# Performance work log

Measured on AMD Instinct MI355X. Metric: run time of the kernel, lower is better.

The kernel has to match this reference:

```python
import jax, jax.numpy as jnp
import numpy as np

BN_EPS = 1e-5
K_HOPS = 10


def setup_inputs() -> dict:
    key = jax.random.key(0)
    ks = jax.random.split(key, 8)
    N, F, H, C, E = 169343, 128, 256, 40, 1200000
    return {
        "x": jax.random.normal(ks[0], (N, F), dtype=jnp.float32),
        "edge_index": jax.random.randint(ks[1], (2, E), 0, N, dtype=jnp.int64),
        "norm": jax.random.uniform(ks[2], (E,), dtype=jnp.float32),
        "W1": jax.random.normal(ks[3], (F, H), dtype=jnp.float32) * (1.0 / np.sqrt(F)),
        "b1": jnp.zeros((H,), jnp.float32),
        "bn_gamma": jnp.ones((H,), jnp.float32),
        "bn_beta": jnp.zeros((H,), jnp.float32),
        "bn_mean": jnp.zeros((H,), jnp.float32),
        "bn_var": jnp.ones((H,), jnp.float32),
        "W2": jax.random.normal(ks[4], (H, C), dtype=jnp.float32) * (1.0 / np.sqrt(H)),
        "b2": jnp.zeros((C,), jnp.float32),
        "proj_w": jax.random.normal(ks[5], (C,), dtype=jnp.float32) * (1.0 / np.sqrt(C)),
        "proj_b": jnp.zeros((1,), jnp.float32),
    }


def reference(x, edge_index, norm, W1, b1, bn_gamma, bn_beta, bn_mean, bn_var,
              W2, b2, proj_w, proj_b):
    N = x.shape[0]
    src, dst = edge_index[0], edge_index[1]

    # MLP head: Linear -> BatchNorm (eval, running stats) -> ReLU -> Linear
    h = x @ W1 + b1
    h = (h - bn_mean) * jax.lax.rsqrt(bn_var + BN_EPS) * bn_gamma + bn_beta
    h = jax.nn.relu(h)  # dropout: identity at inference
    h = h @ W2 + b2  # [N, C]

    # K-hop norm-weighted scatter-add propagation, collecting snapshots
    def hop(carry, _):
        msgs = norm[:, None] * carry[src]              # [E, C]
        nxt = jax.ops.segment_sum(msgs, dst, num_segments=N)
        return nxt, nxt

    _, hops = jax.lax.scan(hop, h, None, length=K_HOPS)  # [K, N, C]
    pps = jnp.concatenate([h[None], hops], axis=0)       # [K+1, N, C]
    pps = jnp.transpose(pps, (1, 0, 2))                  # [N, K+1, C]

    # sigmoid attention over hops, weighted combine
    retain = jax.nn.sigmoid(pps @ proj_w + proj_b[0])    # [N, K+1]
    out = jnp.einsum("nk,nkc->nc", retain, pps)          # [N, C]
    return jax.nn.log_softmax(out, axis=1)
```

## Files before the change

### kernel.cpp

```cpp
#include <hip/hip_runtime.h>
#include <hip/hip_bf16.h>
#include <math.h>

#define F 128
#define H 256
#define C 40
#define KHOPS 10
#define TM 32
#define HK 64

__global__ void k_count(const int* __restrict__ dst, int E, int* __restrict__ cnt) {
    int e = blockIdx.x * 256 + threadIdx.x;
    if (e < E) atomicAdd(&cnt[dst[e]], 1);
}

__global__ void k_scan1(const int* __restrict__ cnt, int n, int* __restrict__ bsum) {
    __shared__ int sh[256];
    int t = threadIdx.x;
    int base = blockIdx.x * 4096 + t * 16;
    int s = 0;
    for (int i = 0; i < 16; i++) { int idx = base + i; if (idx < n) s += cnt[idx]; }
    sh[t] = s; __syncthreads();
    for (int o = 128; o > 0; o >>= 1) {
        if (t < o) sh[t] += sh[t + o];
        __syncthreads();
    }
    if (t == 0) bsum[blockIdx.x] = sh[0];
}

__global__ void k_scan2(int* __restrict__ bsum, int nb) {
    if (threadIdx.x == 0) {
        int acc = 0;
        for (int i = 0; i < nb; i++) { int v = bsum[i]; bsum[i] = acc; acc += v; }
    }
}

__global__ void k_scan3(const int* __restrict__ cnt, int n, const int* __restrict__ bsum,
                        int* __restrict__ rp) {
    __shared__ int sh[256];
    int t = threadIdx.x;
    int base = blockIdx.x * 4096 + t * 16;
    int local[16]; int s = 0;
    for (int i = 0; i < 16; i++) {
        int idx = base + i;
        int v = (idx < n) ? cnt[idx] : 0;
        local[i] = v; s += v;
    }
    sh[t] = s; __syncthreads();
    for (int o = 1; o < 256; o <<= 1) {
        int v = (t >= o) ? sh[t - o] : 0;
        __syncthreads();
        sh[t] += v;
        __syncthreads();
    }
    int excl = (t == 0) ? 0 : sh[t - 1];
    int run = bsum[blockIdx.x] + excl;
    for (int i = 0; i < 16; i++) {
        int idx = base + i;
        if (idx < n) { rp[idx] = run; run += local[i]; }
    }
}

__global__ void k_fill(const int* __restrict__ src, const int* __restrict__ dst,
                       const float* __restrict__ nrm, int E, const int* __restrict__ rp,
                       int* __restrict__ cur, int2* __restrict__ ep) {
    int e = blockIdx.x * 256 + threadIdx.x;
    if (e < E) {
        int d = dst[e];
        int p = rp[d] + atomicAdd(&cur[d], 1);
        ep[p] = make_int2(src[e], __float_as_int(nrm[e]));
    }
}

__launch_bounds__(256, 4)
__global__ void k_mlp(const float* __restrict__ x, const float* __restrict__ W1,
                      const float* __restrict__ b1, const float* __restrict__ g,
                      const float* __restrict__ be, const float* __restrict__ mu,
                      const float* __restrict__ var, const float* __restrict__ W2,
                      const float* __restrict__ b2, const float* __restrict__ pw,
                      const float* __restrict__ pb,
                      float* __restrict__ hbuf, float* __restrict__ oacc, int N) {
    __shared__ float xs[TM][132];
    __shared__ float h1s[TM][68];
    __shared__ float w2s[C][68];
    __shared__ float asc[HK], dsc[HK];
    __shared__ float redc[256];
    __shared__ float sigv[TM];

    int t = threadIdx.x;
    int n0 = blockIdx.x * TM;

    for (int k = 0; k < 4; k++) {
        int idx = k * 256 + t;
        int node = idx >> 5, f4 = idx & 31;
        int n = n0 + node;
        float4 v = (n < N) ? ((const float4*)x)[(size_t)n * (F / 4) + f4]
                           : make_float4(0.f, 0.f, 0.f, 0.f);
        *((float4*)&xs[node][f4 * 4]) = v;
    }

    int n_loc = t >> 3, cg = t & 7;
    float acc2[5];
    #pragma unroll
    for (int j = 0; j < 5; j++) acc2[j] = b2[cg * 5 + j];

    int tn = t & 15, th = t >> 4;
    const float4* W1g = (const float4*)W1;

    for (int h0 = 0; h0 < H; h0 += HK) {
        for (int k = 0; k < 10; k++) {
            int idx = k * 256 + t;
            int hh = idx / 40, c = idx % 40;
            w2s[c][hh] = W2[(size_t)(h0 + hh) * C + c];
        }
        if (t < HK) {
            int hg = h0 + t;
            float a = g[hg] * rsqrtf(var[hg] + 1e-5f);
            asc[t] = a;
            dsc[t] = (b1[hg] - mu[hg]) * a + be[hg];
        }
        __syncthreads();

        float acc[2][4];
        #pragma unroll
        for (int i = 0; i < 2; i++)
            #pragma unroll
            for (int j = 0; j < 4; j++) acc[i][j] = 0.f;

        #pragma unroll 4
        for (int f0 = 0; f0 < F; f0 += 4) {
            float4 wv[4];
            #pragma unroll
            for (int q = 0; q < 4; q++)
                wv[q] = W1g[(size_t)(f0 + q) * (H / 4) + (h0 >> 2) + th];
            float4 xv[2];
            #pragma unroll
            for (int i = 0; i < 2; i++)
                xv[i] = *((const float4*)&xs[tn + 16 * i][f0]);
            #pragma unroll
            for (int i = 0; i < 2; i++) {
                float xa[4] = {xv[i].x, xv[i].y, xv[i].z, xv[i].w};
                #pragma unroll
                for (int q = 0; q < 4; q++) {
                    float wa[4] = {wv[q].x, wv[q].y, wv[q].z, wv[q].w};
                    #pragma unroll
                    for (int j = 0; j < 4; j++) acc[i][j] += xa[q] * wa[j];
                }
            }
        }
        #pragma unroll
        for (int i = 0; i < 2; i++) {
            float4 o;
            float* po = (float*)&o;
            #pragma unroll
            for (int j = 0; j < 4; j++) {
                int hh = th * 4 + j;
                float v = acc[i][j] * asc[hh] + dsc[hh];
                po[j] = v > 0.f ? v : 0.f;
            }
            *((float4*)&h1s[tn + 16 * i][th * 4]) = o;
        }
        __syncthreads();

        #pragma unroll 4
        for (int hh = 0; hh < HK; hh += 4) {
            float4 hv = *((const float4*)&h1s[n_loc][hh]);
            #pragma unroll
            for (int j = 0; j < 5; j++) {
                float4 w4 = *((const float4*)&w2s[cg * 5 + j][hh]);
                acc2[j] += hv.x * w4.x + hv.y * w4.y + hv.z * w4.z + hv.w * w4.w;
            }
        }
        __syncthreads();
    }

    #pragma unroll
    for (int j = 0; j < 5; j++) h1s[n_loc][cg * 5 + j] = acc2[j];
    float part = 0.f;
    #pragma unroll
    for (int j = 0; j < 5; j++) part += acc2[j] * pw[cg * 5 + j];
    redc[t] = part;
    __syncthreads();
    if (cg == 0) {
        float s = 0.f;
        #pragma unroll
        for (int q = 0; q < 8; q++) s += redc[n_loc * 8 + q];
        sigv[n_loc] = 1.f / (1.f + expf(-(s + pb[0])));
    }
    __syncthreads();
    if (t < 160) {
        int row = t / 5, p = t % 5;
        int n = n0 + row;
        if (n < N) {
            float4 a, b;
            a.x = h1s[row][8 * p + 0]; a.y = h1s[row][8 * p + 1];
            a.z = h1s[row][8 * p + 2]; a.w = h1s[row][8 * p + 3];
            b.x = h1s[row][8 * p + 4]; b.y = h1s[row][8 * p + 5];
            b.z = h1s[row][8 * p + 6]; b.w = h1s[row][8 * p + 7];
            float4* hp = (float4*)(hbuf + (size_t)n * C + 8 * p);
            hp[0] = a; hp[1] = b;
            float sg = sigv[row];
            float4 oa, ob;
            oa.x = sg * a.x; oa.y = sg * a.y; oa.z = sg * a.z; oa.w = sg * a.w;
            ob.x = sg * b.x; ob.y = sg * b.y; ob.z = sg * b.z; ob.w = sg * b.w;
            float4* op = (float4*)(oacc + (size_t)n * C + 8 * p);
            op[0] = oa; op[1] = ob;
        }
    }
}

__global__ void k_hop(const float4* __restrict__ cur4, float4* __restrict__ nxt4,
                      float4* __restrict__ oacc4, const int* __restrict__ rp,
                      const int2* __restrict__ ep,
                      const float* __restrict__ pw, const float* __restrict__ pb, int N) {
    __shared__ float red[320];
    __shared__ float sig[64];
    int t = threadIdx.x;
    int nl = t / 5, p = t % 5;
    int n = blockIdx.x * 64 + nl;
    int c0 = 2 * p;
    float4 a0 = make_float4(0.f, 0.f, 0.f, 0.f);
    float4 a1 = make_float4(0.f, 0.f, 0.f, 0.f);
    if (n < N) {
        int b = rp[n], e = rp[n + 1];
        int j = b;
        for (; j + 4 <= e; j += 4) {
            int2 e0 = ep[j], e1 = ep[j + 1], e2 = ep[j + 2], e3 = ep[j + 3];
            const float4* r0 = cur4 + (size_t)e0.x * 10 + c0;
            const float4* r1 = cur4 + (size_t)e1.x * 10 + c0;
            const float4* r2 = cur4 + (size_t)e2.x * 10 + c0;
            const float4* r3 = cur4 + (size_t)e3.x * 10 + c0;
            float4 v00 = r0[0], v01 = r0[1];
            float4 v10 = r1[0], v11 = r1[1];
            float4 v20 = r2[0], v21 = r2[1];
            float4 v30 = r3[0], v31 = r3[1];
            float w0 = __int_as_float(e0.y), w1 = __int_as_float(e1.y);
            float w2 = __int_as_float(e2.y), w3 = __int_as_float(e3.y);
            a0.x += w0 * v00.x; a0.y += w0 * v00.y; a0.z += w0 * v00.z; a0.w += w0 * v00.w;
            a1.x += w0 * v01.x; a1.y += w0 * v01.y; a1.z += w0 * v01.z; a1.w += w0 * v01.w;
            a0.x += w1 * v10.x; a0.y += w1 * v10.y; a0.z += w1 * v10.z; a0.w += w1 * v10.w;
            a1.x += w1 * v11.x; a1.y += w1 * v11.y; a1.z += w1 * v11.z; a1.w += w1 * v11.w;
            a0.x += w2 * v20.x; a0.y += w2 * v20.y; a0.z += w2 * v20.z; a0.w += w2 * v20.w;
            a1.x += w2 * v21.x; a1.y += w2 * v21.y; a1.z += w2 * v21.z; a1.w += w2 * v21.w;
            a0.x += w3 * v30.x; a0.y += w3 * v30.y; a0.z += w3 * v30.z; a0.w += w3 * v30.w;
            a1.x += w3 * v31.x; a1.y += w3 * v31.y; a1.z += w3 * v31.z; a1.w += w3 * v31.w;
        }
        if (j + 2 <= e) {
            int2 e0 = ep[j], e1 = ep[j + 1];
            const float4* r0 = cur4 + (size_t)e0.x * 10 + c0;
            const float4* r1 = cur4 + (size_t)e1.x * 10 + c0;
            float4 v00 = r0[0], v01 = r0[1];
            float4 v10 = r1[0], v11 = r1[1];
            float w0 = __int_as_float(e0.y), w1 = __int_as_float(e1.y);
            a0.x += w0 * v00.x; a0.y += w0 * v00.y; a0.z += w0 * v00.z; a0.w += w0 * v00.w;
            a1.x += w0 * v01.x; a1.y += w0 * v01.y; a1.z += w0 * v01.z; a1.w += w0 * v01.w;
            a0.x += w1 * v10.x; a0.y += w1 * v10.y; a0.z += w1 * v10.z; a0.w += w1 * v10.w;
            a1.x += w1 * v11.x; a1.y += w1 * v11.y; a1.z += w1 * v11.z; a1.w += w1 * v11.w;
            j += 2;
        }
        if (j < e) {
            int2 e0 = ep[j];
            const float4* r0 = cur4 + (size_t)e0.x * 10 + c0;
            float4 v00 = r0[0], v01 = r0[1];
            float w0 = __int_as_float(e0.y);
            a0.x += w0 * v00.x; a0.y += w0 * v00.y; a0.z += w0 * v00.z; a0.w += w0 * v00.w;
            a1.x += w0 * v01.x; a1.y += w0 * v01.y; a1.z += w0 * v01.z; a1.w += w0 * v01.w;
        }
        nxt4[(size_t)n * 10 + c0] = a0;
        nxt4[(size_t)n * 10 + c0 + 1] = a1;
    }
    float4 pw0 = ((const float4*)pw)[c0];
    float4 pw1 = ((const float4*)pw)[c0 + 1];
    red[t] = a0.x * pw0.x + a0.y * pw0.y + a0.z * pw0.z + a0.w * pw0.w
           + a1.x * pw1.x + a1.y * pw1.y + a1.z * pw1.z + a1.w * pw1.w;
    __syncthreads();
    if (p == 0) {
        float s = red[t] + red[t + 1] + red[t + 2] + red[t + 3] + red[t + 4];
        sig[nl] = 1.f / (1.f + expf(-(s + pb[0])));
    }
    __syncthreads();
    if (n < N) {
        float sg = sig[nl];
        size_t o = (size_t)n * 10 + c0;
        float4 v0 = oacc4[o], v1 = oacc4[o + 1];
        v0.x += sg * a0.x; v0.y += sg * a0.y; v0.z += sg * a0.z; v0.w += sg * a0.w;
        v1.x += sg * a1.x; v1.y += sg * a1.y; v1.z += sg * a1.z; v1.w += sg * a1.w;
        oacc4[o] = v0;
        oacc4[o + 1] = v1;
    }
}

__global__ void k_lsm(float4* __restrict__ io, int N) {
    __shared__ float red[320];
    __shared__ float statm[32];
    __shared__ float stats[32];
    int t = threadIdx.x;
    int nl = t / 10, c4 = t % 10;
    int n = blockIdx.x * 32 + nl;
    bool ok = n < N;
    float4 v = ok ? io[(size_t)n * 10 + c4] : make_float4(-1e30f, -1e30f, -1e30f, -1e30f);
    red[t] = fmaxf(fmaxf(v.x, v.y), fmaxf(v.z, v.w));
    __syncthreads();
    if (c4 == 0) {
        float m = -1e30f;
        #pragma unroll
        for (int q = 0; q < 10; q++) m = fmaxf(m, red[nl * 10 + q]);
        statm[nl] = m;
    }
    __syncthreads();
    float m = statm[nl];
    float e0 = expf(v.x - m), e1 = expf(v.y - m), e2 = expf(v.z - m), e3 = expf(v.w - m);
    red[t] = e0 + e1 + e2 + e3;
    __syncthreads();
    if (c4 == 0) {
        float s = 0.f;
        #pragma unroll
        for (int q = 0; q < 10; q++) s += red[nl * 10 + q];
        stats[nl] = logf(s);
    }
    __syncthreads();
    if (ok) {
        float ls = stats[nl];
        io[(size_t)n * 10 + c4] = make_float4(v.x - m - ls, v.y - m - ls, v.z - m - ls, v.w - m - ls);
    }
}

extern "C" void kernel_launch(void* const* d_in, const int* in_sizes, int n_in,
                              void* d_out, int out_size, void* d_ws, size_t ws_size,
                              hipStream_t stream) {
    const float* x   = (const float*)d_in[0];
    const int*   ei  = (const int*)d_in[1];
    const float* nrm = (const float*)d_in[2];
    const float* W1  = (const float*)d_in[3];
    const float* b1  = (const float*)d_in[4];
    const float* g   = (const float*)d_in[5];
    const float* be  = (const float*)d_in[6];
    const float* mu  = (const float*)d_in[7];
    const float* var = (const float*)d_in[8];
    const float* W2  = (const float*)d_in[9];
    const float* b2  = (const float*)d_in[10];
    const float* pw  = (const float*)d_in[11];
    const float* pb  = (const float*)d_in[12];
    float* out = (float*)d_out;

    int N = in_sizes[0] / F;
    int E = in_sizes[2];

    char* w = (char*)d_ws;
    auto alloc = [&](size_t bytes) {
        void* p = (void*)w;
        w += ((bytes + 255) / 256) * 256;
        return p;
    };
    int*   rp     = (int*)alloc((size_t)(N + 1) * 4);
    int*   cursor = (int*)alloc((size_t)(N + 1) * 4);
    int*   bsum   = (int*)alloc(1024);
    int2*  ep     = (int2*)alloc((size_t)E * 8);
    float* bufA   = (float*)alloc((size_t)N * C * 4);
    float* bufB   = (float*)alloc((size_t)N * C * 4);

    hipMemsetAsync(cursor, 0, (size_t)(N + 1) * 4, stream);

    k_count<<<(E + 255) / 256, 256, 0, stream>>>(ei + E, E, cursor);

    int n1 = N + 1;
    int NB = (n1 + 4095) / 4096;
    k_scan1<<<NB, 256, 0, stream>>>(cursor, n1, bsum);
    k_scan2<<<1, 64, 0, stream>>>(bsum, NB);
    k_scan3<<<NB, 256, 0, stream>>>(cursor, n1, bsum, rp);

    hipMemsetAsync(cursor, 0, (size_t)(N + 1) * 4, stream);
    k_fill<<<(E + 255) / 256, 256, 0, stream>>>(ei, ei + E, nrm, E, rp, cursor, ep);

    k_mlp<<<(N + TM - 1) / TM, 256, 0, stream>>>(x, W1, b1, g, be, mu, var, W2, b2,
                                                 pw, pb, bufA, out, N);

    int nodeBlocks64 = (N + 63) / 64;
    float* cur = bufA;
    float* nxt = bufB;
    for (int k = 0; k < KHOPS; k++) {
        k_hop<<<nodeBlocks64, 320, 0, stream>>>((const float4*)cur, (float4*)nxt, (float4*)out,
                                                rp, ep, pw, pb, N);
        float* tmp = cur; cur = nxt; nxt = tmp;
    }

    int nodeBlocks32 = (N + 31) / 32;
    k_lsm<<<nodeBlocks32, 320, 0, stream>>>((float4*)out, N);
}
```

Measured before the change: 1.199 ms.

## Compute first MLP layer with split-bf16 MFMA emulating fp32 precision

Replaces the scalar FP32 x@W1 loop with bf16 MFMA instructions, splitting each fp32 operand into three bf16 parts and summing six cross-products to approximate fp32 accuracy. W1 is pre-split and transposed by a new small kernel. The full 256-wide hidden activation now stays in shared memory, so the per-chunk loop only handles W2. This aims to cut the FP32 ALU cost of the dense layer. In exchange it adds split overhead, more shared memory per block and six MFMAs per tile. The MLP is likely a minor share of a runtime dominated by the hops.

```diff
diff --git a/kernel.cpp b/kernel.cpp
--- a/kernel.cpp
+++ b/kernel.cpp
@@ -7,7 +7,21 @@
 #define C 40
 #define KHOPS 10
 #define TM 32
-#define HK 64
+
+typedef short bf16x8 __attribute__((ext_vector_type(8)));
+typedef float f32x4 __attribute__((ext_vector_type(4)));
+
+__device__ __forceinline__ void split3(float v, ushort& s1, ushort& s2, ushort& s3) {
+    unsigned u = __float_as_uint(v);
+    float f1 = __uint_as_float(u & 0xFFFF0000u);
+    s1 = (ushort)(u >> 16);
+    float r = v - f1;
+    unsigned ur = __float_as_uint(r);
+    float f2 = __uint_as_float(ur & 0xFFFF0000u);
+    s2 = (ushort)(ur >> 16);
+    float r2 = r - f2;
+    s3 = (ushort)(__float_as_uint(r2) >> 16);
+}
 
 __global__ void k_count(const int* __restrict__ dst, int E, int* __restrict__ cnt) {
     int e = blockIdx.x * 256 + threadIdx.x;
@@ -72,99 +86,132 @@
     }
 }
 
-__launch_bounds__(256, 4)
-__global__ void k_mlp(const float* __restrict__ x, const float* __restrict__ W1,
+__global__ void k_wsplit(const float* __restrict__ W1, ushort* __restrict__ w1a,
+                         ushort* __restrict__ w1b, ushort* __restrict__ w1c) {
+    int t = blockIdx.x * 256 + threadIdx.x;
+    if (t < F * H) {
+        int h = t / F, f = t % F;
+        ushort a, b, c;
+        split3(W1[(size_t)f * H + h], a, b, c);
+        w1a[t] = a; w1b[t] = b; w1c[t] = c;
+    }
+}
+
+__launch_bounds__(256)
+__global__ void k_mlp(const float* __restrict__ x,
+                      const ushort* __restrict__ w1a, const ushort* __restrict__ w1b,
+                      const ushort* __restrict__ w1c,
                       const float* __restrict__ b1, const float* __restrict__ g,
                       const float* __restrict__ be, const float* __restrict__ mu,
                       const float* __restrict__ var, const float* __restrict__ W2,
                       const float* __restrict__ b2, const float* __restrict__ pw,
                       const float* __restrict__ pb,
                       float* __restrict__ hbuf, float* __restrict__ oacc, int N) {
-    __shared__ float xs[TM][132];
-    __shared__ float h1s[TM][68];
+    __shared__ ushort xsA[TM][136];
+    __shared__ ushort xsB[TM][136];
+    __shared__ ushort xsC[TM][136];
+    __shared__ float h1s[TM][260];
     __shared__ float w2s[C][68];
-    __shared__ float asc[HK], dsc[HK];
+    __shared__ float ascS[H], dscS[H];
     __shared__ float redc[256];
     __shared__ float sigv[TM];
 
     int t = threadIdx.x;
     int n0 = blockIdx.x * TM;
 
-    for (int k = 0; k < 4; k++) {
-        int idx = k * 256 + t;
+    for (int kk = 0; kk < 4; kk++) {
+        int idx = kk * 256 + t;
         int node = idx >> 5, f4 = idx & 31;
         int n = n0 + node;
         float4 v = (n < N) ? ((const float4*)x)[(size_t)n * (F / 4) + f4]
                            : make_float4(0.f, 0.f, 0.f, 0.f);
-        *((float4*)&xs[node][f4 * 4]) = v;
-    }
+        ushort4 pa, pm, pc;
+        split3(v.x, pa.x, pm.x, pc.x);
+        split3(v.y, pa.y, pm.y, pc.y);
+        split3(v.z, pa.z, pm.z, pc.z);
+        split3(v.w, pa.w, pm.w, pc.w);
+        *((ushort4*)&xsA[node][f4 * 4]) = pa;
+        *((ushort4*)&xsB[node][f4 * 4]) = pm;
+        *((ushort4*)&xsC[node][f4 * 4]) = pc;
+    }
+    {
+        float a = g[t] * rsqrtf(var[t] + 1e-5f);
+        ascS[t] = a;
+        dscS[t] = (b1[t] - mu[t]) * a + be[t];
+    }
+    __syncthreads();
+
+    int lane = t & 63, wv = t >> 6, quad = lane >> 4, lq = lane & 15;
+    int n0w = wv * 64;
+    f32x4 acc[2][4];
+    #pragma unroll
+    for (int mi = 0; mi < 2; mi++)
+        #pragma unroll
+        for (int ni = 0; ni < 4; ni++)
+            acc[mi][ni] = (f32x4){0.f, 0.f, 0.f, 0.f};
+
+    #pragma unroll
+    for (int ks = 0; ks < 4; ks++) {
+        int k0 = ks * 32 + quad * 8;
+        bf16x8 a1[2], a2[2], a3[2];
+        #pragma unroll
+        for (int mi = 0; mi < 2; mi++) {
+            int row = mi * 16 + lq;
+            a1[mi] = *((const bf16x8*)&xsA[row][k0]);
+            a2[mi] = *((const bf16x8*)&xsB[row][k0]);
+            a3[mi] = *((const bf16x8*)&xsC[row][k0]);
+        }
+        #pragma unroll
+        for (int ni = 0; ni < 4; ni++) {
+            size_t wo = (size_t)(n0w + ni * 16 + lq) * F + k0;
+            bf16x8 q1 = *((const bf16x8*)(w1a + wo));
+            bf16x8 q2 = *((const bf16x8*)(w1b + wo));
+            bf16x8 q3 = *((const bf16x8*)(w1c + wo));
+            #pragma unroll
+            for (int mi = 0; mi < 2; mi++) {
+                acc[mi][ni] = __builtin_amdgcn_mfma_f32_16x16x32_bf16(a1[mi], q1, acc[mi][ni], 0, 0, 0);
+                acc[mi][ni] = __builtin_amdgcn_mfma_f32_16x16x32_bf16(a1[mi], q2, acc[mi][ni], 0, 0, 0);
+                acc[mi][ni] = __builtin_amdgcn_mfma_f32_16x16x32_bf16(a2[mi], q1, acc[mi][ni], 0, 0, 0);
+                acc[mi][ni] = __builtin_amdgcn_mfma_f32_16x16x32_bf16(a1[mi], q3, acc[mi][ni], 0, 0, 0);
+                acc[mi][ni] = __builtin_amdgcn_mfma_f32_16x16x32_bf16(a2[mi], q2, acc[mi][ni], 0, 0, 0);
+                acc[mi][ni] = __builtin_amdgcn_mfma_f32_16x16x32_bf16(a3[mi], q1, acc[mi][ni], 0, 0, 0);
+            }
+        }
+    }
+
+    #pragma unroll
+    for (int ni = 0; ni < 4; ni++) {
+        int h = n0w + ni * 16 + lq;
+        float a = ascS[h], d = dscS[h];
+        #pragma unroll
+        for (int mi = 0; mi < 2; mi++) {
+            #pragma unroll
+            for (int r = 0; r < 4; r++) {
+                int node = mi * 16 + quad * 4 + r;
+                float v = acc[mi][ni][r] * a + d;
+                h1s[node][h] = v > 0.f ? v : 0.f;
+            }
+        }
+    }
+    __syncthreads();
 
     int n_loc = t >> 3, cg = t & 7;
     float acc2[5];
     #pragma unroll
     for (int j = 0; j < 5; j++) acc2[j] = b2[cg * 5 + j];
 
-    int tn = t & 15, th = t >> 4;
-    const float4* W1g = (const float4*)W1;
-
-    for (int h0 = 0; h0 < H; h0 += HK) {
-        for (int k = 0; k < 10; k++) {
-            int idx = k * 256 + t;
-            int hh = idx / 40, c = idx % 40;
-            w2s[c][hh] = W2[(size_t)(h0 + hh) * C + c];
-        }
-        if (t < HK) {
-            int hg = h0 + t;
-            float a = g[hg] * rsqrtf(var[hg] + 1e-5f);
-            asc[t] = a;
-            dsc[t] = (b1[hg] - mu[hg]) * a + be[hg];
+    for (int h0 = 0; h0 < H; h0 += 64) {
+        for (int kk = 0; kk < 10; kk++) {
+            int idx = kk * 256 + t;
+            if (idx < 2560) {
+                int hh = idx / 40, c = idx % 40;
+                w2s[c][hh] = W2[(size_t)(h0 + hh) * C + c];
+            }
         }
         __syncthreads();
-
-        float acc[2][4];
-        #pragma unroll
-        for (int i = 0; i < 2; i++)
-            #pragma unroll
-            for (int j = 0; j < 4; j++) acc[i][j] = 0.f;
-
         #pragma unroll 4
-        for (int f0 = 0; f0 < F; f0 += 4) {
-            float4 wv[4];
-            #pragma unroll
-            for (int q = 0; q < 4; q++)
-                wv[q] = W1g[(size_t)(f0 + q) * (H / 4) + (h0 >> 2) + th];
-            float4 xv[2];
-            #pragma unroll
-            for (int i = 0; i < 2; i++)
-                xv[i] = *((const float4*)&xs[tn + 16 * i][f0]);
-            #pragma unroll
-            for (int i = 0; i < 2; i++) {
-                float xa[4] = {xv[i].x, xv[i].y, xv[i].z, xv[i].w};
-                #pragma unroll
-                for (int q = 0; q < 4; q++) {
-                    float wa[4] = {wv[q].x, wv[q].y, wv[q].z, wv[q].w};
-                    #pragma unroll
-                    for (int j = 0; j < 4; j++) acc[i][j] += xa[q] * wa[j];
-                }
-            }
-        }
-        #pragma unroll
-        for (int i = 0; i < 2; i++) {
-            float4 o;
-            float* po = (float*)&o;
-            #pragma unroll
-            for (int j = 0; j < 4; j++) {
-                int hh = th * 4 + j;
-                float v = acc[i][j] * asc[hh] + dsc[hh];
-                po[j] = v > 0.f ? v : 0.f;
-            }
-            *((float4*)&h1s[tn + 16 * i][th * 4]) = o;
-        }
-        __syncthreads();
-
-        #pragma unroll 4
-        for (int hh = 0; hh < HK; hh += 4) {
-            float4 hv = *((const float4*)&h1s[n_loc][hh]);
+        for (int hh = 0; hh < 64; hh += 4) {
+            float4 hv = *((const float4*)&h1s[n_loc][h0 + hh]);
             #pragma unroll
             for (int j = 0; j < 5; j++) {
                 float4 w4 = *((const float4*)&w2s[cg * 5 + j][hh]);
@@ -352,12 +399,15 @@
         w += ((bytes + 255) / 256) * 256;
         return p;
     };
-    int*   rp     = (int*)alloc((size_t)(N + 1) * 4);
-    int*   cursor = (int*)alloc((size_t)(N + 1) * 4);
-    int*   bsum   = (int*)alloc(1024);
-    int2*  ep     = (int2*)alloc((size_t)E * 8);
-    float* bufA   = (float*)alloc((size_t)N * C * 4);
-    float* bufB   = (float*)alloc((size_t)N * C * 4);
+    int*    rp     = (int*)alloc((size_t)(N + 1) * 4);
+    int*    cursor = (int*)alloc((size_t)(N + 1) * 4);
+    int*    bsum   = (int*)alloc(1024);
+    int2*   ep     = (int2*)alloc((size_t)E * 8);
+    ushort* w1a    = (ushort*)alloc((size_t)F * H * 2);
+    ushort* w1b    = (ushort*)alloc((size_t)F * H * 2);
+    ushort* w1c    = (ushort*)alloc((size_t)F * H * 2);
+    float*  bufA   = (float*)alloc((size_t)N * C * 4);
+    float*  bufB   = (float*)alloc((size_t)N * C * 4);
 
     hipMemsetAsync(cursor, 0, (size_t)(N + 1) * 4, stream);
 
@@ -372,8 +422,10 @@
     hipMemsetAsync(cursor, 0, (size_t)(N + 1) * 4, stream);
     k_fill<<<(E + 255) / 256, 256, 0, stream>>>(ei, ei + E, nrm, E, rp, cursor, ep);
 
-    k_mlp<<<(N + TM - 1) / TM, 256, 0, stream>>>(x, W1, b1, g, be, mu, var, W2, b2,
-                                                 pw, pb, bufA, out, N);
+    k_wsplit<<<(F * H + 255) / 256, 256, 0, stream>>>(W1, w1a, w1b, w1c);
+
+    k_mlp<<<(N + TM - 1) / TM, 256, 0, stream>>>(x, w1a, w1b, w1c, b1, g, be, mu, var,
+                                                 W2, b2, pw, pb, bufA, out, N);
 
     int nodeBlocks64 = (N + 63) / 64;
     float* cur = bufA;
```

Result: faster. 1.050 ms (-12.4%).
